# Kernel optimization log

Hardware: AMD Instinct MI355X
Metric: run time of the kernel (lower is better)

## Reference

```python
import jax, jax.numpy as jnp
import numpy as np

POOL = 14
NUM_ROIS = 512
H, W, C = 200, 200, 1024


def setup_inputs() -> dict:
    key = jax.random.key(0)
    k1, k2, k3, k4, k5 = jax.random.split(key, 5)
    img = jax.random.normal(k1, (1, H, W, C), dtype=jnp.float32)
    # valid boxes: x + w <= W, y + h <= H, w,h >= 8
    x = jax.random.randint(k2, (1, NUM_ROIS), 0, W // 2)
    y = jax.random.randint(k3, (1, NUM_ROIS), 0, H // 2)
    w = jax.random.randint(k4, (1, NUM_ROIS), 8, W // 2)
    h = jax.random.randint(k5, (1, NUM_ROIS), 8, H // 2)
    rois = jnp.stack([x, y, w, h], axis=-1).astype(jnp.int32)  # [1, R, 4]
    return {"img": img, "rois": rois}


def _roi_resize(fm, box):
    # fm: [H, W, C]; box: [4] int32 (x, y, w, h)
    x, y, w, h = box[0], box[1], box[2], box[3]
    # TF1 tf.image.resize_images bilinear, align_corners=False (asymmetric):
    # src = dst * (in_size / out_size), taps floored + clamped to crop extent.
    sy = jnp.arange(POOL, dtype=jnp.float32) * (h.astype(jnp.float32) / POOL)
    sx = jnp.arange(POOL, dtype=jnp.float32) * (w.astype(jnp.float32) / POOL)
    y0 = jnp.floor(sy).astype(jnp.int32)
    x0 = jnp.floor(sx).astype(jnp.int32)
    y0c = jnp.clip(y0, 0, h - 1)
    y1c = jnp.clip(y0 + 1, 0, h - 1)
    x0c = jnp.clip(x0, 0, w - 1)
    x1c = jnp.clip(x0 + 1, 0, w - 1)
    wy = (sy - y0.astype(jnp.float32))[:, None, None]  # [P,1,1]
    wx = (sx - x0.astype(jnp.float32))[None, :, None]  # [1,P,1]
    iy0, iy1 = y + y0c, y + y1c  # absolute row indices
    ix0, ix1 = x + x0c, x + x1c  # absolute col indices
    g00 = fm[iy0[:, None], ix0[None, :]]  # [P,P,C]
    g01 = fm[iy0[:, None], ix1[None, :]]
    g10 = fm[iy1[:, None], ix0[None, :]]
    g11 = fm[iy1[:, None], ix1[None, :]]
    top = g00 + (g01 - g00) * wx
    bot = g10 + (g11 - g10) * wx
    return top + (bot - top) * wy


def reference(img, rois):
    fm = img[0]  # [H, W, C]
    out = jax.vmap(lambda b: _roi_resize(fm, b))(rois[0])  # [R, P, P, C]
    return out[None]  # [1, R, P, P, C]
```

## Files before the change

### kernel.cpp

```cpp
#include <hip/hip_runtime.h>

#define POOL 14
#define NUM_ROIS 512
#define IMG_H 200
#define IMG_W 200
#define IMG_C 1024

__global__ __launch_bounds__(256) void roi_bilinear_kernel(
    const float* __restrict__ img,
    const int*   __restrict__ rois,
    float*       __restrict__ out)
{
    const int cell = blockIdx.x;
    const int r    = cell / (POOL * POOL);
    const int pp   = cell - r * (POOL * POOL);
    const int py   = pp / POOL;
    const int px   = pp - py * POOL;

    const int bx = rois[r * 4 + 0];
    const int by = rois[r * 4 + 1];
    const int bw = rois[r * 4 + 2];
    const int bh = rois[r * 4 + 3];

    const float sy = (float)py * ((float)bh / (float)POOL);
    const float sx = (float)px * ((float)bw / (float)POOL);
    const int y0 = (int)floorf(sy);
    const int x0 = (int)floorf(sx);
    const float wy = sy - (float)y0;
    const float wx = sx - (float)x0;

    const int y0c = min(max(y0, 0), bh - 1);
    const int y1c = min(max(y0 + 1, 0), bh - 1);
    const int x0c = min(max(x0, 0), bw - 1);
    const int x1c = min(max(x0 + 1, 0), bw - 1);

    const int iy0 = by + y0c;
    const int iy1 = by + y1c;
    const int ix0 = bx + x0c;
    const int ix1 = bx + x1c;

    const int c = threadIdx.x * 4;

    const float4 g00 = *(const float4*)(img + ((size_t)iy0 * IMG_W + ix0) * IMG_C + c);
    const float4 g01 = *(const float4*)(img + ((size_t)iy0 * IMG_W + ix1) * IMG_C + c);
    const float4 g10 = *(const float4*)(img + ((size_t)iy1 * IMG_W + ix0) * IMG_C + c);
    const float4 g11 = *(const float4*)(img + ((size_t)iy1 * IMG_W + ix1) * IMG_C + c);

    float4 res;
    {
        float top, bot;
        top = g00.x + (g01.x - g00.x) * wx;
        bot = g10.x + (g11.x - g10.x) * wx;
        res.x = top + (bot - top) * wy;
        top = g00.y + (g01.y - g00.y) * wx;
        bot = g10.y + (g11.y - g10.y) * wx;
        res.y = top + (bot - top) * wy;
        top = g00.z + (g01.z - g00.z) * wx;
        bot = g10.z + (g11.z - g10.z) * wx;
        res.z = top + (bot - top) * wy;
        top = g00.w + (g01.w - g00.w) * wx;
        bot = g10.w + (g11.w - g10.w) * wx;
        res.w = top + (bot - top) * wy;
    }

    *(float4*)(out + (size_t)cell * IMG_C + c) = res;
}

extern "C" void kernel_launch(void* const* d_in, const int* in_sizes, int n_in,
                              void* d_out, int out_size, void* d_ws, size_t ws_size,
                              hipStream_t stream) {
    const float* img  = (const float*)d_in[0];
    const int*   rois = (const int*)d_in[1];
    float*       out  = (float*)d_out;

    const int num_cells = NUM_ROIS * POOL * POOL;
    roi_bilinear_kernel<<<num_cells, 256, 0, stream>>>(img, rois, out);
}
```

Measured before the change: 667.7 us.

## Process one output row per block and map ROIs to XCDs for L2 locality

Each block now computes a full pooled row (14 cells) instead of a single cell, looping over px with unrolled loads. The row base pointers and ROI decode are shared across that loop, and block count drops 14x. Block indices are remapped so that all rows of a ROI land on the same XCD (round-robin dispatch assumed), which keeps overlapping source pixels in one L2. In exchange there are fewer blocks and more work per thread, which lowers parallelism and the number of loads in flight per block.

```diff
diff --git a/kernel.cpp b/kernel.cpp
--- a/kernel.cpp
+++ b/kernel.cpp
@@ -5,49 +5,55 @@
 #define IMG_H 200
 #define IMG_W 200
 #define IMG_C 1024
+#define NUM_XCD 8
 
-__global__ __launch_bounds__(256) void roi_bilinear_kernel(
+__global__ __launch_bounds__(256) void roi_row_kernel(
     const float* __restrict__ img,
     const int*   __restrict__ rois,
     float*       __restrict__ out)
 {
-    const int cell = blockIdx.x;
-    const int r    = cell / (POOL * POOL);
-    const int pp   = cell - r * (POOL * POOL);
-    const int py   = pp / POOL;
-    const int px   = pp - py * POOL;
+    const int b   = blockIdx.x;
+    const int xcd = b & (NUM_XCD - 1);
+    const int s   = b >> 3;
+    const int roi_in = s / POOL;
+    const int py     = s - roi_in * POOL;
+    const int r      = xcd * (NUM_ROIS / NUM_XCD) + roi_in;
 
-    const int bx = rois[r * 4 + 0];
-    const int by = rois[r * 4 + 1];
-    const int bw = rois[r * 4 + 2];
-    const int bh = rois[r * 4 + 3];
+    const int4 box = ((const int4*)rois)[r];
+    const int bx = box.x, by = box.y, bw = box.z, bh = box.w;
 
-    const float sy = (float)py * ((float)bh / (float)POOL);
-    const float sx = (float)px * ((float)bw / (float)POOL);
-    const int y0 = (int)floorf(sy);
-    const int x0 = (int)floorf(sx);
+    const float stepy = (float)bh / (float)POOL;
+    const float stepx = (float)bw / (float)POOL;
+
+    const float sy = (float)py * stepy;
+    const int   y0 = (int)floorf(sy);
     const float wy = sy - (float)y0;
-    const float wx = sx - (float)x0;
-
     const int y0c = min(max(y0, 0), bh - 1);
     const int y1c = min(max(y0 + 1, 0), bh - 1);
-    const int x0c = min(max(x0, 0), bw - 1);
-    const int x1c = min(max(x0 + 1, 0), bw - 1);
 
-    const int iy0 = by + y0c;
-    const int iy1 = by + y1c;
-    const int ix0 = bx + x0c;
-    const int ix1 = bx + x1c;
+    const float* __restrict__ row0 = img + (size_t)(by + y0c) * IMG_W * IMG_C;
+    const float* __restrict__ row1 = img + (size_t)(by + y1c) * IMG_W * IMG_C;
 
     const int c = threadIdx.x * 4;
+    float* __restrict__ orow =
+        out + ((size_t)r * (POOL * POOL) + (size_t)py * POOL) * IMG_C + c;
 
-    const float4 g00 = *(const float4*)(img + ((size_t)iy0 * IMG_W + ix0) * IMG_C + c);
-    const float4 g01 = *(const float4*)(img + ((size_t)iy0 * IMG_W + ix1) * IMG_C + c);
-    const float4 g10 = *(const float4*)(img + ((size_t)iy1 * IMG_W + ix0) * IMG_C + c);
-    const float4 g11 = *(const float4*)(img + ((size_t)iy1 * IMG_W + ix1) * IMG_C + c);
+#pragma unroll
+    for (int px = 0; px < POOL; ++px) {
+        const float sx = (float)px * stepx;
+        const int   x0 = (int)floorf(sx);
+        const float wx = sx - (float)x0;
+        const int x0c = min(max(x0, 0), bw - 1);
+        const int x1c = min(max(x0 + 1, 0), bw - 1);
+        const int ix0 = bx + x0c;
+        const int ix1 = bx + x1c;
 
-    float4 res;
-    {
+        const float4 g00 = *(const float4*)(row0 + (size_t)ix0 * IMG_C + c);
+        const float4 g01 = *(const float4*)(row0 + (size_t)ix1 * IMG_C + c);
+        const float4 g10 = *(const float4*)(row1 + (size_t)ix0 * IMG_C + c);
+        const float4 g11 = *(const float4*)(row1 + (size_t)ix1 * IMG_C + c);
+
+        float4 res;
         float top, bot;
         top = g00.x + (g01.x - g00.x) * wx;
         bot = g10.x + (g11.x - g10.x) * wx;
@@ -61,9 +67,9 @@
         top = g00.w + (g01.w - g00.w) * wx;
         bot = g10.w + (g11.w - g10.w) * wx;
         res.w = top + (bot - top) * wy;
+
+        *(float4*)(orow + (size_t)px * IMG_C) = res;
     }
-
-    *(float4*)(out + (size_t)cell * IMG_C + c) = res;
 }
 
 extern "C" void kernel_launch(void* const* d_in, const int* in_sizes, int n_in,
@@ -73,6 +79,6 @@
     const int*   rois = (const int*)d_in[1];
     float*       out  = (float*)d_out;
 
-    const int num_cells = NUM_ROIS * POOL * POOL;
-    roi_bilinear_kernel<<<num_cells, 256, 0, stream>>>(img, rois, out);
+    const int num_blocks = NUM_ROIS * POOL;
+    roi_row_kernel<<<num_blocks, 256, 0, stream>>>(img, rois, out);
 }
```

Result: faster. 633.8 us (-5.1%).
